# Kernel optimization log

Hardware: AMD Instinct MI355X
Metric: run time of the kernel (lower is better)

The kernel has to match this reference:

```python
import jax, jax.numpy as jnp
import numpy as np

N = 25000        # nodes
E = 400000       # edges (avg degree 16)
F_IN = 256       # input node feature dim
C = 32           # tensor-product channels (linear_1 output)
A = 9            # spherical-harmonic dim (lmax=2)
WNUM = C * A     # per-edge TP weight numel (_head_weight_numel)
B = 8            # radial basis size (edge embedding)
H = 64           # edge MLP hidden width
S = 4            # species (node_attrs one-hot width)
F_OUT = 256      # output node feature dim
AVG_NEIGH = 16.0


def setup_inputs() -> dict:
    key = jax.random.key(0)
    ks = jax.random.split(key, 11)
    sc = lambda fan: np.float32(1.0 / np.sqrt(fan))
    return {
        "x": jax.random.normal(ks[0], (N, F_IN), jnp.float32),
        "node_attrs": jax.random.uniform(ks[1], (N, S), jnp.float32),
        "edge_embedding": jax.random.uniform(ks[2], (E, B), jnp.float32),
        "edge_attr": jax.random.normal(ks[3], (E, A), jnp.float32),
        "edge_index": jax.random.randint(ks[4], (2, E), 0, N, jnp.int32),
        "W1": jax.random.normal(ks[5], (F_IN, C), jnp.float32) * sc(F_IN),
        "Wm1": jax.random.normal(ks[6], (B, H), jnp.float32) * sc(B),
        "Wm2": jax.random.normal(ks[7], (H, H), jnp.float32) * sc(H),
        "Wm3": jax.random.normal(ks[8], (H, WNUM), jnp.float32) * sc(H),
        "W2": jax.random.normal(ks[9], (WNUM, F_OUT), jnp.float32) * sc(WNUM),
        "Wsc": jax.random.normal(ks[10], (F_IN, S, F_OUT), jnp.float32) * sc(F_IN * S),
    }


def reference(x, node_attrs, edge_embedding, edge_attr, edge_index,
              W1, Wm1, Wm2, Wm3, W2, Wsc):
    # self-connection: FullyConnectedTensorProduct(x, node_attrs) -> [N, F_OUT]
    sc_out = jnp.einsum('nf,ns,fso->no', x, node_attrs, Wsc)

    # linear_1 + avg-neighbor normalization -> [N, C]
    h = (x @ W1) * (1.0 / jnp.sqrt(jnp.asarray(AVG_NEIGH, x.dtype)))

    # edge MLP on radial embedding -> per-edge TP weights [E, C, A]
    w = jax.nn.silu(edge_embedding @ Wm1)
    w = jax.nn.silu(w @ Wm2)
    w = (w @ Wm3).reshape(E, C, A)

    edge_dst = edge_index[0]
    edge_src = edge_index[1]

    # gather-TP-scatter: msg[e,c,a] = w[e,c,a] * h[src[e],c] * sh[e,a]
    msg = w * h[edge_src][:, :, None] * edge_attr[:, None, :]   # [E, C, A]
    agg = jax.ops.segment_sum(msg.reshape(E, WNUM), edge_dst,
                              num_segments=N)                    # [N, C*A]

    # linear_2 + activation + self-connection
    out = jax.nn.silu(agg @ W2) + sc_out                         # [N, F_OUT]
    return out
```

## Files before the change

kernel.cpp:

```cpp
#include <hip/hip_runtime.h>

#define NN   25000
#define EE   400000
#define FIN  256
#define CC   32
#define AA   9
#define WN   288
#define BB   8
#define HH   64
#define SS   4
#define FOUT 256
#define EPB  32

typedef float f32x4 __attribute__((ext_vector_type(4)));
typedef short short8 __attribute__((ext_vector_type(8)));

__device__ __forceinline__ float silu_f(float v){ return v / (1.0f + __expf(-v)); }

__device__ __forceinline__ unsigned short f2bf(float f){
  unsigned int u = __builtin_bit_cast(unsigned int, f);
  u += 0x7FFFu + ((u >> 16) & 1u);
  return (unsigned short)(u >> 16);
}

__global__ __launch_bounds__(256) void k_h(const float* __restrict__ x,
                                           const float* __restrict__ W1,
                                           float* __restrict__ h){
  int gid = blockIdx.x * 256 + threadIdx.x;
  int n = gid >> 5, c = gid & 31;
  const float* xr = x + (size_t)n * FIN;
  float acc = 0.f;
  #pragma unroll 8
  for (int f = 0; f < FIN; ++f) acc = fmaf(xr[f], W1[f * CC + c], acc);
  h[gid] = acc * 0.25f;
}

__global__ __launch_bounds__(256) void k_cvt(const float* __restrict__ Wm1,
                                             const float* __restrict__ Wm2,
                                             const float* __restrict__ Wm3,
                                             unsigned short* __restrict__ wm1t,
                                             unsigned short* __restrict__ wm2t,
                                             unsigned short* __restrict__ wm3t){
  int i = blockIdx.x * 256 + threadIdx.x;
  if (i < HH * 32){
    int n = i >> 5, k = i & 31;
    wm1t[i] = (k < BB) ? f2bf(Wm1[k * HH + n]) : (unsigned short)0;
  }
  if (i < HH * HH){
    int n = i >> 6, k = i & 63;
    wm2t[n * 64 + k] = f2bf(Wm2[k * HH + n]);
  }
  if (i < WN * HH){
    int n = i >> 6, k = i & 63;
    wm3t[n * 64 + k] = f2bf(Wm3[k * WN + n]);
  }
}

__global__ __launch_bounds__(256) void k_cvtsc(const float* __restrict__ Wsc,
                                               unsigned short* __restrict__ wscb){
  __shared__ float tile[32][33];
  const int k0 = blockIdx.x * 32;
  const int n0 = blockIdx.y * 32;
  const int t = threadIdx.x;
  #pragma unroll
  for (int p = 0; p < 4; ++p){
    int idx = t + p * 256;
    int r = idx >> 5, c = idx & 31;
    tile[r][c] = Wsc[(size_t)(k0 + r) * 256 + n0 + c];
  }
  __syncthreads();
  #pragma unroll
  for (int p = 0; p < 4; ++p){
    int idx = t + p * 256;
    int r = idx >> 5, c = idx & 31;
    wscb[(size_t)(n0 + r) * 1024 + k0 + c] = f2bf(tile[c][r]);
  }
}

__global__ __launch_bounds__(256) void k_hist(const int* __restrict__ eidx,
                                              int* __restrict__ cnt){
  int e = blockIdx.x * 256 + threadIdx.x;
  if (e < EE) atomicAdd(&cnt[eidx[e]], 1);
}

__global__ __launch_bounds__(1024) void k_scan(const int* __restrict__ cnt,
                                               int* __restrict__ cur){
  __shared__ int part[1024];
  const int t = threadIdx.x;
  const int base = t * 25;
  int s = 0;
  for (int i = 0; i < 25; ++i){
    int idx = base + i;
    s += (idx < NN) ? cnt[idx] : 0;
  }
  part[t] = s;
  __syncthreads();
  for (int off = 1; off < 1024; off <<= 1){
    int v = (t >= off) ? part[t - off] : 0;
    __syncthreads();
    part[t] += v;
    __syncthreads();
  }
  int run = part[t] - s;
  for (int i = 0; i < 25; ++i){
    int idx = base + i;
    if (idx < NN){
      cur[idx] = run;
      run += cnt[idx];
    }
  }
}

__global__ __launch_bounds__(256) void k_scatter(const int* __restrict__ eidx,
                                                 const float* __restrict__ eemb,
                                                 const float* __restrict__ sh,
                                                 int* __restrict__ cur,
                                                 unsigned short* __restrict__ ee_p,
                                                 float* __restrict__ sh_p,
                                                 int* __restrict__ src_p,
                                                 int* __restrict__ dst_p){
  int e = blockIdx.x * 256 + threadIdx.x;
  if (e < EE){
    int d = eidx[e];
    int p = atomicAdd(&cur[d], 1);
    dst_p[p] = d;
    src_p[p] = eidx[EE + e];
    float4 v0 = *(const float4*)&eemb[(size_t)e * BB];
    float4 v1 = *(const float4*)&eemb[(size_t)e * BB + 4];
    unsigned short t[8] = {f2bf(v0.x), f2bf(v0.y), f2bf(v0.z), f2bf(v0.w),
                           f2bf(v1.x), f2bf(v1.y), f2bf(v1.z), f2bf(v1.w)};
    *(short8*)&ee_p[(size_t)p * BB] = *(short8*)t;
    #pragma unroll
    for (int a = 0; a < AA; ++a) sh_p[(size_t)p * AA + a] = sh[(size_t)e * AA + a];
  }
}

__global__ __launch_bounds__(256) void k_sc(const float* __restrict__ x,
                                            const float* __restrict__ na,
                                            const unsigned short* __restrict__ wscb,
                                            float* __restrict__ out){
  __shared__ __align__(16) unsigned short As[64][72];
  __shared__ __align__(16) unsigned short Bs[256][72];
  const int tid = threadIdx.x;
  const int m0 = blockIdx.x * 64;
  const int sm = tid >> 2;
  const int sq = tid & 3;
  float4 nav = {0.f, 0.f, 0.f, 0.f};
  if (m0 + sm < NN) nav = *(const float4*)&na[(size_t)(m0 + sm) * SS];
  const float nf[4] = {nav.x, nav.y, nav.z, nav.w};
  const int lane = tid & 63, wv = tid >> 6;
  const int row = lane & 15, kg = lane >> 4;
  const f32x4 zf = {0.f, 0.f, 0.f, 0.f};
  f32x4 acc[16];
  #pragma unroll
  for (int i = 0; i < 16; ++i) acc[i] = zf;

  for (int kc = 0; kc < FIN * SS; kc += 64){
    __syncthreads();
    {
      float4 xv = {0.f, 0.f, 0.f, 0.f};
      int fc4 = (kc >> 2) + sq * 4;
      if (m0 + sm < NN) xv = *(const float4*)&x[(size_t)(m0 + sm) * FIN + fc4];
      float xf[4] = {xv.x, xv.y, xv.z, xv.w};
      unsigned short tmp[16];
      #pragma unroll
      for (int f = 0; f < 4; ++f)
        #pragma unroll
        for (int s = 0; s < 4; ++s) tmp[f * 4 + s] = f2bf(xf[f] * nf[s]);
      *(short8*)&As[sm][sq * 16]     = *(short8*)&tmp[0];
      *(short8*)&As[sm][sq * 16 + 8] = *(short8*)&tmp[8];
    }
    #pragma unroll
    for (int r = 0; r < 4; ++r){
      int ch = tid + r * 256;
      int n = ch >> 2, c4 = ch & 3;
      const unsigned short* src = wscb + (size_t)n * 1024 + kc + c4 * 16;
      *(short8*)&Bs[n][c4 * 16]     = *(const short8*)src;
      *(short8*)&Bs[n][c4 * 16 + 8] = *(const short8*)(src + 8);
    }
    __syncthreads();
    #pragma unroll
    for (int ks = 0; ks < 2; ++ks){
      short8 af = *(const short8*)&As[wv * 16 + row][ks * 32 + kg * 8];
      #pragma unroll
      for (int nt = 0; nt < 16; ++nt){
        short8 bfr = *(const short8*)&Bs[nt * 16 + row][ks * 32 + kg * 8];
        acc[nt] = __builtin_amdgcn_mfma_f32_16x16x32_bf16(af, bfr, acc[nt], 0, 0, 0);
      }
    }
  }
  #pragma unroll
  for (int nt = 0; nt < 16; ++nt){
    #pragma unroll
    for (int r = 0; r < 4; ++r){
      int m = m0 + wv * 16 + kg * 4 + r;
      if (m < NN) out[(size_t)m * FOUT + nt * 16 + row] = acc[nt][r];
    }
  }
}

__global__ __launch_bounds__(128) void k_edge(const unsigned short* __restrict__ ee_p,
                                              const float* __restrict__ sh_p,
                                              const int* __restrict__ src_p,
                                              const int* __restrict__ dst_p,
                                              const float* __restrict__ h,
                                              const unsigned short* __restrict__ wm1t,
                                              const unsigned short* __restrict__ wm2t,
                                              const unsigned short* __restrict__ wm3t,
                                              float* __restrict__ agg){
  __shared__ float sh_s[EPB][13];
  __shared__ float hs_s[EPB][36];
  __shared__ __align__(16) char scratch[8 * WN * 4];
  __shared__ int   dst_s[EPB];
  __shared__ unsigned char dloc_s[EPB];
  __shared__ unsigned char firstE_s[8];
  __shared__ int   nD_s;
  unsigned short (*t1b)[72] = (unsigned short(*)[72])scratch;
  unsigned short (*t2b)[72] = (unsigned short(*)[72])(scratch + 4608);
  float (*agg_s)[WN] = (float(*)[WN])scratch;
  const int tid = threadIdx.x;

  const int nwg = EE / EPB;
  const int q = nwg >> 3, rr = nwg & 7;
  int bid = blockIdx.x;
  int xcd = bid & 7, li = bid >> 3;
  int swz = (xcd < rr ? xcd * (q + 1) : rr * (q + 1) + (xcd - rr) * q) + li;
  const int e0 = swz * EPB;

  {
    int e = tid >> 2, c0 = (tid & 3) * 8;
    const float* hr = h + (size_t)src_p[e0 + e] * CC + c0;
    *(float4*)&hs_s[e][c0]     = *(const float4*)hr;
    *(float4*)&hs_s[e][c0 + 4] = *(const float4*)(hr + 4);
  }
  for (int i = tid; i < EPB * AA; i += 128){
    int e = i / 9, a = i - e * 9;
    sh_s[e][a] = sh_p[(size_t)e0 * AA + i];
  }
  if (tid < 8) firstE_s[tid] = 0;
  if (tid < EPB){
    int d = dst_p[e0 + tid];
    dst_s[tid] = d;
    bool bnd = (tid > 0) && (d != dst_p[e0 + tid - 1]);
    unsigned long long m = __ballot(bnd);
    int dl = __popcll(m & ((2ull << tid) - 1ull));
    dloc_s[tid] = (unsigned char)dl;
    if (bnd && dl < 8) firstE_s[dl] = (unsigned char)tid;
    if (tid == EPB - 1) nD_s = dl + 1;
  }
  __syncthreads();

  const int lane = tid & 63;
  const int wv   = tid >> 6;
  const int row  = lane & 15;
  const int kg   = lane >> 4;
  const f32x4 zf = {0.f, 0.f, 0.f, 0.f};

  {
    short8 a1 = {0, 0, 0, 0, 0, 0, 0, 0};
    if (kg == 0) a1 = *(const short8*)&ee_p[(size_t)(e0 + wv * 16 + row) * BB];
    #pragma unroll
    for (int nt = 0; nt < 4; ++nt){
      short8 b = *(const short8*)&wm1t[(nt * 16 + row) * 32 + kg * 8];
      f32x4 acc = __builtin_amdgcn_mfma_f32_16x16x32_bf16(a1, b, zf, 0, 0, 0);
      #pragma unroll
      for (int r = 0; r < 4; ++r)
        t1b[wv * 16 + kg * 4 + r][nt * 16 + row] = f2bf(silu_f(acc[r]));
    }
  }

  {
    short8 a2k0 = *(const short8*)&t1b[wv * 16 + row][kg * 8];
    short8 a2k1 = *(const short8*)&t1b[wv * 16 + row][kg * 8 + 32];
    #pragma unroll
    for (int nt = 0; nt < 4; ++nt){
      const unsigned short* bp = wm2t + (size_t)((nt * 16 + row) * 64 + kg * 8);
      short8 b0 = *(const short8*)bp;
      short8 b1 = *(const short8*)(bp + 32);
      f32x4 acc = __builtin_amdgcn_mfma_f32_16x16x32_bf16(a2k0, b0, zf, 0, 0, 0);
      acc = __builtin_amdgcn_mfma_f32_16x16x32_bf16(a2k1, b1, acc, 0, 0, 0);
      #pragma unroll
      for (int r = 0; r < 4; ++r)
        t2b[wv * 16 + kg * 4 + r][nt * 16 + row] = f2bf(silu_f(acc[r]));
    }
  }

  {
    short8 a3k0 = *(const short8*)&t2b[wv * 16 + row][kg * 8];
    short8 a3k1 = *(const short8*)&t2b[wv * 16 + row][kg * 8 + 32];
    const int ebase = wv * 16 + kg * 4;
    int dl[4], d[4];
    #pragma unroll
    for (int r = 0; r < 4; ++r){ dl[r] = dloc_s[ebase + r]; d[r] = dst_s[ebase + r]; }
    const int nD = nD_s;
    const bool direct = (nD > 8);
    __syncthreads();
    if (!direct){
      for (int i = tid; i < nD * WN; i += 128) ((float*)agg_s)[i] = 0.f;
    }
    __syncthreads();

    int c  = (row >= 9) ? 1 : 0;
    int a_ = row - 9 * c;
    const unsigned short* bp = wm3t + (size_t)(row * 64 + kg * 8);
    short8 b0n = *(const short8*)bp;
    short8 b1n = *(const short8*)(bp + 32);
    for (int nt = 0; nt < 18; ++nt){
      short8 b0 = b0n, b1 = b1n;
      if (nt < 17){
        const unsigned short* bp2 = wm3t + (size_t)(((nt + 1) * 16 + row) * 64 + kg * 8);
        b0n = *(const short8*)bp2;
        b1n = *(const short8*)(bp2 + 32);
      }
      f32x4 acc = __builtin_amdgcn_mfma_f32_16x16x32_bf16(a3k0, b0, zf, 0, 0, 0);
      acc = __builtin_amdgcn_mfma_f32_16x16x32_bf16(a3k1, b1, acc, 0, 0, 0);
      int j = nt * 16 + row;
      float vals[4];
      #pragma unroll
      for (int r = 0; r < 4; ++r)
        vals[r] = acc[r] * hs_s[ebase + r][c] * sh_s[ebase + r][a_];
      #pragma unroll
      for (int r = 0; r < 4; ++r){
        bool last = (r == 3) || (dl[r + 1] != dl[r]);
        if (!last){
          vals[r + 1] += vals[r];
        } else if (direct){
          atomicAdd(&agg[(size_t)d[r] * WN + j], vals[r]);
        } else {
          atomicAdd(&agg_s[dl[r]][j], vals[r]);
        }
      }
      a_ += 7; c += 1;
      if (a_ >= 9){ a_ -= 9; c += 1; }
    }

    __syncthreads();
    if (!direct){
      for (int l = 0; l < nD; ++l){
        int dd = dst_s[firstE_s[l]];
        float* dstp = &agg[(size_t)dd * WN];
        if (l > 0 && l < nD - 1){
          for (int j = tid; j < WN; j += 128) dstp[j] = agg_s[l][j];
        } else {
          for (int j = tid; j < WN; j += 128) atomicAdd(&dstp[j], agg_s[l][j]);
        }
      }
    }
  }
}

__global__ __launch_bounds__(256) void k_out(const float* __restrict__ agg,
                                             const float* __restrict__ W2,
                                             float* __restrict__ out){
  __shared__ float As[32][68];
  __shared__ float Bs[32][64];
  const int row0 = blockIdx.x * 64;
  const int col0 = blockIdx.y * 64;
  const int tid = threadIdx.x;
  const int tm = tid >> 4, tn = tid & 15;
  float acc[4][4] = {};
  for (int kc = 0; kc < WN; kc += 32){
    #pragma unroll
    for (int t = 0; t < 8; ++t){
      int idx = tid + t * 256;
      int m = idx >> 5, kk = idx & 31;
      int n = row0 + m;
      float v = 0.f;
      if (n < NN) v = agg[(size_t)n * WN + kc + kk];
      As[kk][m] = v;
    }
    #pragma unroll
    for (int t = 0; t < 8; ++t){
      int idx = tid + t * 256;
      int o = idx & 63, kk = idx >> 6;
      Bs[kk][o] = W2[(size_t)(kc + kk) * FOUT + col0 + o];
    }
    __syncthreads();
    #pragma unroll
    for (int kk = 0; kk < 32; ++kk){
      float4 av = *(const float4*)&As[kk][tm * 4];
      float4 bv = *(const float4*)&Bs[kk][tn * 4];
      float a[4] = {av.x, av.y, av.z, av.w};
      float b[4] = {bv.x, bv.y, bv.z, bv.w};
      #pragma unroll
      for (int i = 0; i < 4; ++i)
        #pragma unroll
        for (int j = 0; j < 4; ++j)
          acc[i][j] = fmaf(a[i], b[j], acc[i][j]);
    }
    __syncthreads();
  }
  #pragma unroll
  for (int i = 0; i < 4; ++i){
    int n = row0 + tm * 4 + i;
    if (n < NN){
      float4 sc = *(const float4*)&out[(size_t)n * FOUT + col0 + tn * 4];
      float4 v;
      v.x = silu_f(acc[i][0]) + sc.x;
      v.y = silu_f(acc[i][1]) + sc.y;
      v.z = silu_f(acc[i][2]) + sc.z;
      v.w = silu_f(acc[i][3]) + sc.w;
      *(float4*)&out[(size_t)n * FOUT + col0 + tn * 4] = v;
    }
  }
}

extern "C" void kernel_launch(void* const* d_in, const int* in_sizes, int n_in,
                              void* d_out, int out_size, void* d_ws, size_t ws_size,
                              hipStream_t stream){
  const float* x    = (const float*)d_in[0];
  const float* na   = (const float*)d_in[1];
  const float* eemb = (const float*)d_in[2];
  const float* shp  = (const float*)d_in[3];
  const int*   eidx = (const int*)d_in[4];
  const float* W1   = (const float*)d_in[5];
  const float* Wm1  = (const float*)d_in[6];
  const float* Wm2  = (const float*)d_in[7];
  const float* Wm3  = (const float*)d_in[8];
  const float* W2   = (const float*)d_in[9];
  const float* Wsc  = (const float*)d_in[10];
  float* out  = (float*)d_out;

  float* agg  = (float*)d_ws;
  float* hbuf = agg + (size_t)NN * WN;
  float* sh_p = hbuf + (size_t)NN * CC;
  int*   cnt  = (int*)(sh_p + (size_t)EE * AA);
  int*   cur  = cnt + NN;
  int*   src_p = cur + NN;
  int*   dst_p = src_p + EE;
  unsigned short* ee_p = (unsigned short*)(dst_p + EE);
  unsigned short* wm1t = ee_p + (size_t)EE * BB;
  unsigned short* wm2t = wm1t + HH * 32;
  unsigned short* wm3t = wm2t + HH * HH;
  unsigned short* wscb = wm3t + WN * HH;

  hipMemsetAsync(agg, 0, (size_t)NN * WN * sizeof(float), stream);
  hipMemsetAsync(cnt, 0, (size_t)NN * sizeof(int), stream);
  k_cvt    <<<dim3((WN * HH + 255) / 256), dim3(256), 0, stream>>>(Wm1, Wm2, Wm3, wm1t, wm2t, wm3t);
  k_cvtsc  <<<dim3(32, 8), dim3(256), 0, stream>>>(Wsc, wscb);
  k_hist   <<<dim3((EE + 255) / 256), dim3(256),  0, stream>>>(eidx, cnt);
  k_scan   <<<dim3(1),                dim3(1024), 0, stream>>>(cnt, cur);
  k_scatter<<<dim3((EE + 255) / 256), dim3(256),  0, stream>>>(eidx, eemb, shp, cur,
                                                               ee_p, sh_p, src_p, dst_p);
  k_h  <<<dim3(NN * CC / 256), dim3(256), 0, stream>>>(x, W1, hbuf);
  k_sc <<<dim3((NN + 63) / 64), dim3(256), 0, stream>>>(x, na, wscb, out);
  k_edge<<<dim3(EE / EPB), dim3(128), 0, stream>>>(ee_p, sh_p, src_p, dst_p, hbuf,
                                                   wm1t, wm2t, wm3t, agg);
  k_out<<<dim3((NN + 63) / 64, FOUT / 64), dim3(256), 0, stream>>>(agg, W2, out);
}
```

Before: 587.1 us.

## Double edges per block in k_edge and transpose gathered h/sh tiles

Each k_edge block now handles 64 edges with 256 threads instead of 32 with 128, and up to 10 local destination segments are staged in shared memory. This is meant to cut global atomics at segment boundaries and amortise the per-block setup. The gathered h and spherical-harmonic values are stored transposed in shared memory, so each lane fetches its four edges with one vector read instead of scalar strided reads. One barrier is dropped, and the two MLP activation buffers now share the same shared-memory region, which relies on each wave only touching its own rows. The larger blocks reduce block count and may lower occupancy.

```diff
diff --git a/kernel.cpp b/kernel.cpp
--- a/kernel.cpp
+++ b/kernel.cpp
@@ -10,7 +10,8 @@
 #define HH   64
 #define SS   4
 #define FOUT 256
-#define EPB  32
+#define EPB  64
+#define NSEG 10
 
 typedef float f32x4 __attribute__((ext_vector_type(4)));
 typedef short short8 __attribute__((ext_vector_type(8)));
@@ -199,7 +200,7 @@
   }
 }
 
-__global__ __launch_bounds__(128) void k_edge(const unsigned short* __restrict__ ee_p,
+__global__ __launch_bounds__(256) void k_edge(const unsigned short* __restrict__ ee_p,
                                               const float* __restrict__ sh_p,
                                               const int* __restrict__ src_p,
                                               const int* __restrict__ dst_p,
@@ -208,15 +209,15 @@
                                               const unsigned short* __restrict__ wm2t,
                                               const unsigned short* __restrict__ wm3t,
                                               float* __restrict__ agg){
-  __shared__ float sh_s[EPB][13];
-  __shared__ float hs_s[EPB][36];
-  __shared__ __align__(16) char scratch[8 * WN * 4];
+  __shared__ float hs_t[CC][EPB];
+  __shared__ float sh_t[AA][EPB];
+  __shared__ __align__(16) char scratch[NSEG * WN * 4];
   __shared__ int   dst_s[EPB];
   __shared__ unsigned char dloc_s[EPB];
-  __shared__ unsigned char firstE_s[8];
+  __shared__ unsigned char firstE_s[NSEG];
   __shared__ int   nD_s;
   unsigned short (*t1b)[72] = (unsigned short(*)[72])scratch;
-  unsigned short (*t2b)[72] = (unsigned short(*)[72])(scratch + 4608);
+  unsigned short (*t2b)[72] = t1b;
   float (*agg_s)[WN] = (float(*)[WN])scratch;
   const int tid = threadIdx.x;
 
@@ -230,14 +231,18 @@
   {
     int e = tid >> 2, c0 = (tid & 3) * 8;
     const float* hr = h + (size_t)src_p[e0 + e] * CC + c0;
-    *(float4*)&hs_s[e][c0]     = *(const float4*)hr;
-    *(float4*)&hs_s[e][c0 + 4] = *(const float4*)(hr + 4);
-  }
-  for (int i = tid; i < EPB * AA; i += 128){
+    float4 v0 = *(const float4*)hr;
+    float4 v1 = *(const float4*)(hr + 4);
+    hs_t[c0 + 0][e] = v0.x; hs_t[c0 + 1][e] = v0.y;
+    hs_t[c0 + 2][e] = v0.z; hs_t[c0 + 3][e] = v0.w;
+    hs_t[c0 + 4][e] = v1.x; hs_t[c0 + 5][e] = v1.y;
+    hs_t[c0 + 6][e] = v1.z; hs_t[c0 + 7][e] = v1.w;
+  }
+  for (int i = tid; i < EPB * AA; i += 256){
     int e = i / 9, a = i - e * 9;
-    sh_s[e][a] = sh_p[(size_t)e0 * AA + i];
-  }
-  if (tid < 8) firstE_s[tid] = 0;
+    sh_t[a][e] = sh_p[(size_t)e0 * AA + i];
+  }
+  if (tid < NSEG) firstE_s[tid] = 0;
   if (tid < EPB){
     int d = dst_p[e0 + tid];
     dst_s[tid] = d;
@@ -245,10 +250,9 @@
     unsigned long long m = __ballot(bnd);
     int dl = __popcll(m & ((2ull << tid) - 1ull));
     dloc_s[tid] = (unsigned char)dl;
-    if (bnd && dl < 8) firstE_s[dl] = (unsigned char)tid;
+    if (bnd && dl < NSEG) firstE_s[dl] = (unsigned char)tid;
     if (tid == EPB - 1) nD_s = dl + 1;
   }
-  __syncthreads();
 
   const int lane = tid & 63;
   const int wv   = tid >> 6;
@@ -289,14 +293,16 @@
     short8 a3k0 = *(const short8*)&t2b[wv * 16 + row][kg * 8];
     short8 a3k1 = *(const short8*)&t2b[wv * 16 + row][kg * 8 + 32];
     const int ebase = wv * 16 + kg * 4;
+
+    __syncthreads();
+
     int dl[4], d[4];
     #pragma unroll
     for (int r = 0; r < 4; ++r){ dl[r] = dloc_s[ebase + r]; d[r] = dst_s[ebase + r]; }
     const int nD = nD_s;
-    const bool direct = (nD > 8);
-    __syncthreads();
+    const bool direct = (nD > NSEG);
     if (!direct){
-      for (int i = tid; i < nD * WN; i += 128) ((float*)agg_s)[i] = 0.f;
+      for (int i = tid; i < nD * WN; i += 256) ((float*)agg_s)[i] = 0.f;
     }
     __syncthreads();
 
@@ -315,10 +321,11 @@
       f32x4 acc = __builtin_amdgcn_mfma_f32_16x16x32_bf16(a3k0, b0, zf, 0, 0, 0);
       acc = __builtin_amdgcn_mfma_f32_16x16x32_bf16(a3k1, b1, acc, 0, 0, 0);
       int j = nt * 16 + row;
+      f32x4 hv = *(const f32x4*)&hs_t[c][ebase];
+      f32x4 sv = *(const f32x4*)&sh_t[a_][ebase];
       float vals[4];
       #pragma unroll
-      for (int r = 0; r < 4; ++r)
-        vals[r] = acc[r] * hs_s[ebase + r][c] * sh_s[ebase + r][a_];
+      for (int r = 0; r < 4; ++r) vals[r] = acc[r] * hv[r] * sv[r];
       #pragma unroll
       for (int r = 0; r < 4; ++r){
         bool last = (r == 3) || (dl[r + 1] != dl[r]);
@@ -340,9 +347,9 @@
         int dd = dst_s[firstE_s[l]];
         float* dstp = &agg[(size_t)dd * WN];
         if (l > 0 && l < nD - 1){
-          for (int j = tid; j < WN; j += 128) dstp[j] = agg_s[l][j];
+          for (int j = tid; j < WN; j += 256) dstp[j] = agg_s[l][j];
         } else {
-          for (int j = tid; j < WN; j += 128) atomicAdd(&dstp[j], agg_s[l][j]);
+          for (int j = tid; j < WN; j += 256) atomicAdd(&dstp[j], agg_s[l][j]);
         }
       }
     }
@@ -444,7 +451,7 @@
                                                                ee_p, sh_p, src_p, dst_p);
   k_h  <<<dim3(NN * CC / 256), dim3(256), 0, stream>>>(x, W1, hbuf);
   k_sc <<<dim3((NN + 63) / 64), dim3(256), 0, stream>>>(x, na, wscb, out);
-  k_edge<<<dim3(EE / EPB), dim3(128), 0, stream>>>(ee_p, sh_p, src_p, dst_p, hbuf,
+  k_edge<<<dim3(EE / EPB), dim3(256), 0, stream>>>(ee_p, sh_p, src_p, dst_p, hbuf,
                                                    wm1t, wm2t, wm3t, agg);
   k_out<<<dim3((NN + 63) / 64, FOUT / 64), dim3(256), 0, stream>>>(agg, W2, out);
 }
```

New measurement: 603.5 us. 2.8% more time.
